# Kernel optimization log

Hardware: AMD Instinct MI355X
Metric: run time of the kernel (lower is better)

Reference implementation:

```python
import jax, jax.numpy as jnp
import numpy as np

BS, SEQ, ENC, DEC, HEADS, INTERM = 32, 2048, 512, 512, 8, 128
IH = INTERM * HEADS


def setup_inputs() -> dict:
    key = jax.random.key(0)
    ks = jax.random.split(key, 16)
    s = 0.02
    return {
        "enc": jax.random.normal(ks[0], (BS, SEQ, ENC), jnp.float32),
        "dec": jax.random.normal(ks[1], (BS, 1, DEC + ENC), jnp.float32),
        "kappa": jax.random.uniform(ks[2], (BS, 1, HEADS), jnp.float32),
        "mask": jnp.ones((BS, SEQ, 1), jnp.float32),
        "Wv": jax.random.normal(ks[3], (ENC, IH), jnp.float32) * s,
        "bv": jnp.zeros((IH,), jnp.float32),
        "Wq": jax.random.normal(ks[4], (DEC + ENC, IH), jnp.float32) * s,
        "bq": jnp.zeros((IH,), jnp.float32),
        "Wf": jax.random.normal(ks[5], (IH, HEADS), jnp.float32) * s,
        "bf": jnp.zeros((HEADS,), jnp.float32),
        "Wb": jax.random.normal(ks[6], (DEC + ENC, HEADS), jnp.float32) * s,
        "bb": jnp.zeros((HEADS,), jnp.float32),
        "Wk": jax.random.normal(ks[7], (DEC + ENC, HEADS), jnp.float32) * s,
        "bk": jnp.zeros((HEADS,), jnp.float32),
        "Wfc": jax.random.normal(ks[8], (ENC * HEADS, ENC), jnp.float32) * s,
        "bfc": jnp.zeros((ENC,), jnp.float32),
    }


def reference(enc, dec, kappa, mask, Wv, bv, Wq, bq, Wf, bf, Wb, bb, Wk, bk, Wfc, bfc):
    bs, seq_len, _ = enc.shape
    sp = jax.nn.softplus
    value = enc @ Wv + bv                      # (bs, seq, IH)
    query = dec @ Wq + bq                      # (bs, 1, IH), broadcasts over seq
    alpha = sp(jnp.tanh(query + value) @ Wf + bf) * mask   # (bs, seq, heads)
    beta = sp(dec @ Wb + bb)                   # (bs, 1, heads)
    kappa = kappa + sp(dec @ Wk + bk)          # (bs, 1, heads)
    u = jnp.arange(seq_len, dtype=enc.dtype)[None, :, None]
    score = alpha * jnp.exp(-beta * (kappa - u) ** 2)       # (bs, seq, heads)
    # weighted reduction over seq: (bs, heads, enc) then flatten in heads-major order
    context = jnp.einsum("bsh,bse->bhe", score, enc).reshape(bs, -1)
    context = context @ Wfc + bfc              # (bs, enc)
    return context[:, None, :], kappa, score
```

## Files before the change

### kernel.cpp

```cpp
#include <hip/hip_runtime.h>
#include <cstdint>
#include <cstddef>

#define BSZ    32
#define SEQL   2048
#define ENCD   512
#define DE     1024
#define NHEADS 8
#define IHD    1024

typedef unsigned short u16;
typedef __bf16 bf16x8 __attribute__((ext_vector_type(8)));
typedef float floatx4 __attribute__((ext_vector_type(4)));
typedef unsigned short u16x8 __attribute__((ext_vector_type(8)));

__device__ __forceinline__ u16 f2bf(float f) {
    unsigned int u = __float_as_uint(f);
    u = (u + 0x7FFFu + ((u >> 16) & 1u)) >> 16;
    return (u16)u;
}
__device__ __forceinline__ float bf2f(u16 v) {
    return __uint_as_float(((unsigned int)v) << 16);
}
__device__ __forceinline__ float softplus_f(float x) {
    return fmaxf(x, 0.0f) + log1pf(__expf(-fabsf(x)));
}
__device__ __forceinline__ float tanh_fast(float x) {
    const float e = __expf(2.0f * x);
    return 1.0f - 2.0f / (e + 1.0f);
}
__device__ __forceinline__ void async_cp16(u16* lds, const u16* g) {
    __builtin_amdgcn_global_load_lds(
        (const __attribute__((address_space(1))) unsigned int*)g,
        (__attribute__((address_space(3))) unsigned int*)lds, 16, 0, 0);
}

__global__ __launch_bounds__(256) void pre_kernel(
    const float* __restrict__ Wv, const float* __restrict__ Wf,
    u16* __restrict__ WvT, u16* __restrict__ wfb,
    const float* __restrict__ dec, const float* __restrict__ kappa_in,
    const float* __restrict__ Wq, const float* __restrict__ bq,
    const float* __restrict__ bv,
    const float* __restrict__ Wb, const float* __restrict__ bb,
    const float* __restrict__ Wk, const float* __restrict__ bk,
    float* __restrict__ query_ws, float* __restrict__ beta_ws,
    float* __restrict__ kappa_out)
{
    __shared__ float sh[64 * 65];
    const int bid = blockIdx.x, tid = threadIdx.x;

    if (bid < 128) {
        const int nt = bid & 15, kt = bid >> 4;
        for (int i = tid; i < 4096; i += 256) {
            const int kk = i >> 6, nn = i & 63;
            sh[kk * 65 + nn] = Wv[(size_t)(kt * 64 + kk) * IHD + nt * 64 + nn];
        }
        __syncthreads();
        for (int i = tid; i < 4096; i += 256) {
            const int nn = i >> 6, kk = i & 63;
            WvT[(size_t)(nt * 64 + nn) * 512 + kt * 64 + kk] = f2bf(sh[kk * 65 + nn]);
        }
        return;
    }
    if (bid == 128) {
        for (int i = tid; i < 8192; i += 256) {
            const int j   = i & 7;
            const int fr8 = (i >> 3) & 7;
            const int qd  = (i >> 6) & 3;
            const int ks  = (i >> 8) & 3;
            const int nn  = i >> 10;
            const int row = nn * 128 + ks * 32 + qd * 8 + j;
            wfb[i] = f2bf(Wf[row * NHEADS + fr8]);
        }
        return;
    }
    const int p = bid - 129;
    const int b = p & 31, y = p >> 5;
    float* s_dec = sh;
    float* s_red = sh + DE;
    for (int i = tid; i < DE; i += 256) s_dec[i] = dec[b * DE + i];
    __syncthreads();

    if (y < 32) {
        const int cl = tid & 31, kg = tid >> 5;
        const int col = y * 32 + cl;
        float a = 0.f;
        const float* w = Wq + col;
        #pragma unroll 4
        for (int k = kg * 128; k < kg * 128 + 128; ++k)
            a = fmaf(s_dec[k], w[(size_t)k * IHD], a);
        s_red[tid] = a;
        __syncthreads();
        if (tid < 32) {
            float s = 0.f;
            #pragma unroll
            for (int i = 0; i < 8; ++i) s += s_red[i * 32 + tid];
            query_ws[(size_t)b * IHD + col] = s + bq[col] + bv[col];
        }
    } else {
        const int h = tid & 7, kg = tid >> 3;
        float ab = 0.f, ak = 0.f;
        for (int k = kg * 32; k < kg * 32 + 32; ++k) {
            const float d = s_dec[k];
            ab = fmaf(d, Wb[k * NHEADS + h], ab);
            ak = fmaf(d, Wk[k * NHEADS + h], ak);
        }
        s_red[tid] = ab;
        __syncthreads();
        for (int off = 128; off >= 8; off >>= 1) {
            if (tid < off) s_red[tid] += s_red[tid + off];
            __syncthreads();
        }
        const float abT = (tid < 8) ? s_red[tid] : 0.f;
        __syncthreads();
        s_red[tid] = ak;
        __syncthreads();
        for (int off = 128; off >= 8; off >>= 1) {
            if (tid < off) s_red[tid] += s_red[tid + off];
            __syncthreads();
        }
        if (tid < 8) {
            beta_ws[b * NHEADS + tid]   = softplus_f(bb[tid] + abT);
            kappa_out[b * NHEADS + tid] = kappa_in[b * NHEADS + tid]
                                        + softplus_f(bk[tid] + s_red[tid]);
        }
    }
}

#define BM 128

__global__ __launch_bounds__(256, 2) void gemm_score_ctx_kernel(
    const float* __restrict__ enc, u16* __restrict__ encb,
    const u16* __restrict__ wvT,
    const u16* __restrict__ wfb2, const float* __restrict__ bf_g,
    const float* __restrict__ mask, const float* __restrict__ query_ws,
    const float* __restrict__ beta_ws, const float* __restrict__ kappa_out,
    float* __restrict__ score_out, float* __restrict__ ctx_part)
{
    __shared__ __align__(16) unsigned char smem[69632];
    u16*   tT      = (u16*)(smem + 32768);
    float* s_score = (float*)(smem + 65536);

    const int tid  = threadIdx.x;
    const int m0   = blockIdx.x * BM;
    const int b    = blockIdx.x >> 4;
    const int sc   = blockIdx.x & 15;
    const int lane = tid & 63;
    const int w    = tid >> 6;
    const int wr   = w >> 1, wc = w & 1;
    const int fr   = lane & 15, quad = lane >> 4;

    {
        const float4* src = (const float4*)enc + (size_t)m0 * 128;
        u16x8* dst = (u16x8*)(encb + (size_t)m0 * 512);
        #pragma unroll 4
        for (int i = tid; i < 8192; i += 256) {
            const float4 a = src[i * 2], b2 = src[i * 2 + 1];
            u16x8 o;
            o[0] = f2bf(a.x);  o[1] = f2bf(a.y);  o[2] = f2bf(a.z);  o[3] = f2bf(a.w);
            o[4] = f2bf(b2.x); o[5] = f2bf(b2.y); o[6] = f2bf(b2.z); o[7] = f2bf(b2.w);
            dst[i] = o;
        }
        asm volatile("s_waitcnt vmcnt(0)" ::: "memory");
        __builtin_amdgcn_sched_barrier(0);
        __builtin_amdgcn_s_barrier();
    }

    int mA[4], csA[4];
    #pragma unroll
    for (int r = 0; r < 4; ++r) {
        const int c = r * 256 + tid;
        mA[r]  = c >> 3;
        csA[r] = (c & 7) ^ (mA[r] & 7);
    }

    auto stage = [&](int bufsel, int it) {
        u16* Ab = (u16*)(smem + bufsel * 32768);
        u16* Bb = Ab + 8192;
        const int nn2 = it >> 3, kt2 = it & 7;
        const size_t aoff = (size_t)kt2 * 64;
        const size_t boff = (size_t)nn2 * (128 * 512) + (size_t)kt2 * 64;
        #pragma unroll
        for (int r = 0; r < 4; ++r) {
            async_cp16(Ab + (r * 256 + (tid & 192)) * 8,
                       encb + (size_t)(m0 + mA[r]) * 512 + aoff + csA[r] * 8);
            async_cp16(Bb + (size_t)(r * 256 + (tid & 192)) * 8,
                       wvT + (size_t)mA[r] * 512 + boff + csA[r] * 8);
        }
    };

    floatx4 acc2[2] = {};

    stage(0, 0);

    for (int nn = 0; nn < 8; ++nn) {
        const int n0 = nn * 128;
        float qv[4];
        bf16x8 wfr[4];
        floatx4 acc[4][4] = {};

        #pragma unroll
        for (int kt = 0; kt < 8; ++kt) {
            const int it = nn * 8 + kt;
            if (kt < 7 || nn < 7)
                stage((it + 1) & 1, it + 1);
            if (kt == 0) {
                #pragma unroll
                for (int nt = 0; nt < 4; ++nt)
                    qv[nt] = query_ws[(size_t)b * IHD + n0 + wc * 64 + nt * 16 + fr];
                #pragma unroll
                for (int ks = 0; ks < 4; ++ks)
                    wfr[ks] = *(const bf16x8*)&wfb2[((nn * 4 + ks) * 4 + quad) * 64
                                                    + (fr & 7) * 8];
            }
            if (kt == 7 && nn == 7) {
                asm volatile("s_waitcnt vmcnt(0)" ::: "memory");
            } else if (kt == 0) {
                asm volatile("s_waitcnt vmcnt(16)" ::: "memory");
            } else {
                asm volatile("s_waitcnt vmcnt(8)" ::: "memory");
            }
            __builtin_amdgcn_sched_barrier(0);
            __builtin_amdgcn_s_barrier();

            u16* Ab = (u16*)(smem + (it & 1) * 32768);
            u16* Bb = Ab + 8192;
            __builtin_amdgcn_s_setprio(1);
            #pragma unroll
            for (int s2 = 0; s2 < 2; ++s2) {
                bf16x8 af[4], bfr[4];
                #pragma unroll
                for (int mt = 0; mt < 4; ++mt) {
                    const int ma = wr * 64 + mt * 16 + fr;
                    const int ca = (s2 * 4 + quad) ^ (ma & 7);
                    af[mt] = *(const bf16x8*)&Ab[ma * 64 + ca * 8];
                }
                #pragma unroll
                for (int nt = 0; nt < 4; ++nt) {
                    const int nb = wc * 64 + nt * 16 + fr;
                    const int cb = (s2 * 4 + quad) ^ (nb & 7);
                    bfr[nt] = *(const bf16x8*)&Bb[nb * 64 + cb * 8];
                }
                #pragma unroll
                for (int mt = 0; mt < 4; ++mt)
                    #pragma unroll
                    for (int nt = 0; nt < 4; ++nt)
                        acc[mt][nt] = __builtin_amdgcn_mfma_f32_16x16x32_bf16(
                            af[mt], bfr[nt], acc[mt][nt], 0, 0, 0);
            }
            __builtin_amdgcn_s_setprio(0);
            __builtin_amdgcn_sched_barrier(0);
            __builtin_amdgcn_s_barrier();
        }

        #pragma unroll
        for (int mt = 0; mt < 4; ++mt) {
            #pragma unroll
            for (int nt = 0; nt < 4; ++nt) {
                const int col = wc * 64 + nt * 16 + fr;
                #pragma unroll
                for (int reg = 0; reg < 4; ++reg) {
                    const int row = wr * 64 + mt * 16 + quad * 4 + reg;
                    ((__bf16*)tT)[row * 128 + (col ^ ((row & 7) << 3))] =
                        (__bf16)tanh_fast(acc[mt][nt][reg] + qv[nt]);
                }
            }
        }
        asm volatile("s_waitcnt lgkmcnt(0)" ::: "memory");
        __builtin_amdgcn_sched_barrier(0);
        __builtin_amdgcn_s_barrier();

        #pragma unroll
        for (int t = 0; t < 2; ++t) {
            const int row = w * 32 + t * 16 + fr;
            #pragma unroll
            for (int ks = 0; ks < 4; ++ks) {
                const bf16x8 ta = *(const bf16x8*)
                    &tT[row * 128 + ((ks * 32 + quad * 8) ^ ((row & 7) << 3))];
                acc2[t] = __builtin_amdgcn_mfma_f32_16x16x32_bf16(ta, wfr[ks], acc2[t], 0, 0, 0);
            }
        }
        __builtin_amdgcn_sched_barrier(0);
        __builtin_amdgcn_s_barrier();
    }

    if (fr < NHEADS) {
        const float bfh = bf_g[fr];
        const float bet = beta_ws[b * NHEADS + fr];
        const float kap = kappa_out[b * NHEADS + fr];
        #pragma unroll
        for (int t = 0; t < 2; ++t) {
            #pragma unroll
            for (int reg = 0; reg < 4; ++reg) {
                const int row  = w * 32 + t * 16 + quad * 4 + reg;
                const int grow = m0 + row;
                const int s = grow & 2047;
                const float alpha = softplus_f(acc2[t][reg] + bfh) * mask[grow];
                const float du = kap - (float)s;
                const float v = alpha * __expf(-bet * du * du);
                score_out[(size_t)grow * NHEADS + fr] = v;
                s_score[row * NHEADS + fr] = v;
            }
        }
    }
    asm volatile("s_waitcnt lgkmcnt(0)" ::: "memory");
    __builtin_amdgcn_s_barrier();

    {
        float acc0[8] = {}, acc1[8] = {};
        const u16* ep = encb + (size_t)m0 * 512 + lane * 8;
        for (int s0 = 0; s0 < 128; s0 += 16) {
            u16x8 ev[16];
            #pragma unroll
            for (int u = 0; u < 16; ++u)
                ev[u] = *(const u16x8*)(ep + (size_t)(s0 + u) * 512);
            #pragma unroll
            for (int u = 0; u < 16; ++u) {
                const float2 sc2 = *(const float2*)&s_score[(s0 + u) * NHEADS + 2 * w];
                #pragma unroll
                for (int j = 0; j < 8; ++j) {
                    const float e = bf2f(ev[u][j]);
                    acc0[j] = fmaf(sc2.x, e, acc0[j]);
                    acc1[j] = fmaf(sc2.y, e, acc1[j]);
                }
            }
        }
        const int e8 = lane * 8;
        float* outp = ctx_part + ((size_t)sc * BSZ + b) * (NHEADS * ENCD);
        *(float4*)&outp[(2 * w + 0) * ENCD + e8]     = make_float4(acc0[0], acc0[1], acc0[2], acc0[3]);
        *(float4*)&outp[(2 * w + 0) * ENCD + e8 + 4] = make_float4(acc0[4], acc0[5], acc0[6], acc0[7]);
        *(float4*)&outp[(2 * w + 1) * ENCD + e8]     = make_float4(acc1[0], acc1[1], acc1[2], acc1[3]);
        *(float4*)&outp[(2 * w + 1) * ENCD + e8 + 4] = make_float4(acc1[4], acc1[5], acc1[6], acc1[7]);
    }
}

__global__ __launch_bounds__(256) void ctx_reduce_kernel(
    const float* __restrict__ part, float* __restrict__ ctx_ws)
{
    const int i = blockIdx.x * 256 + threadIdx.x;
    float a = 0.f;
    #pragma unroll
    for (int sc = 0; sc < 16; ++sc)
        a += part[(size_t)sc * 131072 + i];
    ctx_ws[i] = a;
}

__global__ __launch_bounds__(256) void final_kernel(
    const float* __restrict__ ctx_ws, const float* __restrict__ Wfc,
    const float* __restrict__ bfc, float* __restrict__ out_ctx)
{
    __shared__ float s_ctx[32][128];
    const int jc = blockIdx.x, ks = blockIdx.y, tid = threadIdx.x;
    const int jl = tid & 31, bg = tid >> 5;
    const int j = jc * 32 + jl;
    const int k0 = ks * 128;

    for (int i = tid; i < 32 * 128; i += 256) {
        const int bb2 = i >> 7, kk = i & 127;
        s_ctx[bb2][kk] = ctx_ws[(size_t)bb2 * (NHEADS * ENCD) + k0 + kk];
    }
    __syncthreads();

    float a0 = 0.f, a1 = 0.f, a2 = 0.f, a3 = 0.f;
    for (int kk = 0; kk < 128; ++kk) {
        const float wv = Wfc[(size_t)(k0 + kk) * ENCD + j];
        a0 = fmaf(s_ctx[bg * 4 + 0][kk], wv, a0);
        a1 = fmaf(s_ctx[bg * 4 + 1][kk], wv, a1);
        a2 = fmaf(s_ctx[bg * 4 + 2][kk], wv, a2);
        a3 = fmaf(s_ctx[bg * 4 + 3][kk], wv, a3);
    }
    const float bias = (ks == 0) ? bfc[j] : 0.0f;
    atomicAdd(&out_ctx[(bg * 4 + 0) * ENCD + j], a0 + bias);
    atomicAdd(&out_ctx[(bg * 4 + 1) * ENCD + j], a1 + bias);
    atomicAdd(&out_ctx[(bg * 4 + 2) * ENCD + j], a2 + bias);
    atomicAdd(&out_ctx[(bg * 4 + 3) * ENCD + j], a3 + bias);
}

extern "C" void kernel_launch(void* const* d_in, const int* in_sizes, int n_in,
                              void* d_out, int out_size, void* d_ws, size_t ws_size,
                              hipStream_t stream)
{
    const float* enc   = (const float*)d_in[0];
    const float* dec   = (const float*)d_in[1];
    const float* kapin = (const float*)d_in[2];
    const float* mask  = (const float*)d_in[3];
    const float* Wv    = (const float*)d_in[4];
    const float* bv    = (const float*)d_in[5];
    const float* Wq    = (const float*)d_in[6];
    const float* bq    = (const float*)d_in[7];
    const float* Wf    = (const float*)d_in[8];
    const float* bf    = (const float*)d_in[9];
    const float* Wb    = (const float*)d_in[10];
    const float* bb    = (const float*)d_in[11];
    const float* Wk    = (const float*)d_in[12];
    const float* bk    = (const float*)d_in[13];
    const float* Wfc   = (const float*)d_in[14];
    const float* bfc   = (const float*)d_in[15];

    float* out       = (float*)d_out;
    float* out_ctx   = out;
    float* out_kappa = out + 16384;
    float* out_score = out + 16640;

    char* w = (char*)d_ws;
    u16*   enc_bf   = (u16*)w;
    float* ctx_part = (float*)(w + 67108864);
    u16*   wvT      = (u16*)(w + 75497472);
    float* q_ws     = (float*)(w + 76546048);
    float* beta_ws  = (float*)(w + 76677120);
    float* ctx_ws   = (float*)(w + 76678144);
    u16*   wfb      = (u16*)(w + 77202432);

    hipMemsetAsync(out_ctx, 0, 16384 * sizeof(float), stream);

    pre_kernel<<<dim3(128 + 1 + 1056), dim3(256), 0, stream>>>(
        Wv, Wf, wvT, wfb,
        dec, kapin, Wq, bq, bv, Wb, bb, Wk, bk, q_ws, beta_ws, out_kappa);

    gemm_score_ctx_kernel<<<dim3((BSZ * SEQL) / BM), dim3(256), 0, stream>>>(
        enc, enc_bf, wvT, wfb, bf, mask, q_ws, beta_ws, out_kappa,
        out_score, ctx_part);

    ctx_reduce_kernel<<<dim3(512), dim3(256), 0, stream>>>(ctx_part, ctx_ws);

    final_kernel<<<dim3(16, 32), dim3(256), 0, stream>>>(
        ctx_ws, Wfc, bfc, out_ctx);
}
```

Before: 396.0 us.

## Enlarge fused GEMM block tile to 256x256 with 512 threads

Doubles the per-block M tile to 256 rows and the N chunk to 256 columns, with 8 waves per block and a 4x8 MFMA accumulator tile per wave. LDS grows to about 136KB to hold double-buffered A/B tiles and a 256-row tanh tile. The aim is to reuse each loaded Wv and enc tile across more output and to halve the grid to 256 blocks. The tanh epilogue now runs in two halves, with only one column group of waves writing at a time, and per-thread register pressure rises sharply. The context reduction splits the waves across two 128-row halves so the partial-sum layout stays the same.

```diff
diff --git a/kernel.cpp b/kernel.cpp
--- a/kernel.cpp
+++ b/kernel.cpp
@@ -127,9 +127,9 @@
     }
 }
 
-#define BM 128
-
-__global__ __launch_bounds__(256, 2) void gemm_score_ctx_kernel(
+#define BM 256
+
+__global__ __launch_bounds__(512, 1) void gemm_score_ctx_kernel(
     const float* __restrict__ enc, u16* __restrict__ encb,
     const u16* __restrict__ wvT,
     const u16* __restrict__ wfb2, const float* __restrict__ bf_g,
@@ -137,14 +137,14 @@
     const float* __restrict__ beta_ws, const float* __restrict__ kappa_out,
     float* __restrict__ score_out, float* __restrict__ ctx_part)
 {
-    __shared__ __align__(16) unsigned char smem[69632];
-    u16*   tT      = (u16*)(smem + 32768);
-    float* s_score = (float*)(smem + 65536);
+    __shared__ __align__(16) unsigned char smem[139264];
+    u16*   tT      = (u16*)(smem + 65536);
+    float* s_score = (float*)(smem + 131072);
 
     const int tid  = threadIdx.x;
     const int m0   = blockIdx.x * BM;
-    const int b    = blockIdx.x >> 4;
-    const int sc   = blockIdx.x & 15;
+    const int b    = blockIdx.x >> 3;
+    const int scb  = blockIdx.x & 7;
     const int lane = tid & 63;
     const int w    = tid >> 6;
     const int wr   = w >> 1, wc = w & 1;
@@ -154,7 +154,7 @@
         const float4* src = (const float4*)enc + (size_t)m0 * 128;
         u16x8* dst = (u16x8*)(encb + (size_t)m0 * 512);
         #pragma unroll 4
-        for (int i = tid; i < 8192; i += 256) {
+        for (int i = tid; i < 16384; i += 512) {
             const float4 a = src[i * 2], b2 = src[i * 2 + 1];
             u16x8 o;
             o[0] = f2bf(a.x);  o[1] = f2bf(a.y);  o[2] = f2bf(a.z);  o[3] = f2bf(a.w);
@@ -169,66 +169,50 @@
     int mA[4], csA[4];
     #pragma unroll
     for (int r = 0; r < 4; ++r) {
-        const int c = r * 256 + tid;
+        const int c = r * 512 + tid;
         mA[r]  = c >> 3;
         csA[r] = (c & 7) ^ (mA[r] & 7);
     }
 
-    auto stage = [&](int bufsel, int it) {
-        u16* Ab = (u16*)(smem + bufsel * 32768);
-        u16* Bb = Ab + 8192;
-        const int nn2 = it >> 3, kt2 = it & 7;
+    auto stage = [&](int sel, int pp2, int kt2) {
+        u16* Ab = (u16*)(smem + sel * 65536);
+        u16* Bb = Ab + 16384;
         const size_t aoff = (size_t)kt2 * 64;
-        const size_t boff = (size_t)nn2 * (128 * 512) + (size_t)kt2 * 64;
+        const size_t boff = (size_t)pp2 * (256 * 512) + (size_t)kt2 * 64;
         #pragma unroll
         for (int r = 0; r < 4; ++r) {
-            async_cp16(Ab + (r * 256 + (tid & 192)) * 8,
+            async_cp16(Ab + (r * 512 + (tid & 448)) * 8,
                        encb + (size_t)(m0 + mA[r]) * 512 + aoff + csA[r] * 8);
-            async_cp16(Bb + (size_t)(r * 256 + (tid & 192)) * 8,
+            async_cp16(Bb + (size_t)(r * 512 + (tid & 448)) * 8,
                        wvT + (size_t)mA[r] * 512 + boff + csA[r] * 8);
         }
     };
 
     floatx4 acc2[2] = {};
 
-    stage(0, 0);
-
-    for (int nn = 0; nn < 8; ++nn) {
-        const int n0 = nn * 128;
-        float qv[4];
-        bf16x8 wfr[4];
-        floatx4 acc[4][4] = {};
+    stage(0, 0, 0);
+
+    for (int pp = 0; pp < 4; ++pp) {
+        floatx4 acc[4][8] = {};
 
         #pragma unroll
         for (int kt = 0; kt < 8; ++kt) {
-            const int it = nn * 8 + kt;
-            if (kt < 7 || nn < 7)
-                stage((it + 1) & 1, it + 1);
-            if (kt == 0) {
-                #pragma unroll
-                for (int nt = 0; nt < 4; ++nt)
-                    qv[nt] = query_ws[(size_t)b * IHD + n0 + wc * 64 + nt * 16 + fr];
-                #pragma unroll
-                for (int ks = 0; ks < 4; ++ks)
-                    wfr[ks] = *(const bf16x8*)&wfb2[((nn * 4 + ks) * 4 + quad) * 64
-                                                    + (fr & 7) * 8];
-            }
-            if (kt == 7 && nn == 7) {
+            if (kt < 7)       stage((kt + 1) & 1, pp, kt + 1);
+            else if (pp < 3)  stage(0, pp + 1, 0);
+            if (kt == 7 && pp == 3) {
                 asm volatile("s_waitcnt vmcnt(0)" ::: "memory");
-            } else if (kt == 0) {
-                asm volatile("s_waitcnt vmcnt(16)" ::: "memory");
             } else {
                 asm volatile("s_waitcnt vmcnt(8)" ::: "memory");
             }
             __builtin_amdgcn_sched_barrier(0);
             __builtin_amdgcn_s_barrier();
 
-            u16* Ab = (u16*)(smem + (it & 1) * 32768);
-            u16* Bb = Ab + 8192;
+            const u16* Ab = (const u16*)(smem + (kt & 1) * 65536);
+            const u16* Bb = Ab + 16384;
             __builtin_amdgcn_s_setprio(1);
             #pragma unroll
             for (int s2 = 0; s2 < 2; ++s2) {
-                bf16x8 af[4], bfr[4];
+                bf16x8 af[4], bfr[8];
                 #pragma unroll
                 for (int mt = 0; mt < 4; ++mt) {
                     const int ma = wr * 64 + mt * 16 + fr;
@@ -236,15 +220,15 @@
                     af[mt] = *(const bf16x8*)&Ab[ma * 64 + ca * 8];
                 }
                 #pragma unroll
-                for (int nt = 0; nt < 4; ++nt) {
-                    const int nb = wc * 64 + nt * 16 + fr;
+                for (int nt = 0; nt < 8; ++nt) {
+                    const int nb = wc * 128 + nt * 16 + fr;
                     const int cb = (s2 * 4 + quad) ^ (nb & 7);
                     bfr[nt] = *(const bf16x8*)&Bb[nb * 64 + cb * 8];
                 }
                 #pragma unroll
                 for (int mt = 0; mt < 4; ++mt)
                     #pragma unroll
-                    for (int nt = 0; nt < 4; ++nt)
+                    for (int nt = 0; nt < 8; ++nt)
                         acc[mt][nt] = __builtin_amdgcn_mfma_f32_16x16x32_bf16(
                             af[mt], bfr[nt], acc[mt][nt], 0, 0, 0);
             }
@@ -254,34 +238,50 @@
         }
 
         #pragma unroll
-        for (int mt = 0; mt < 4; ++mt) {
-            #pragma unroll
-            for (int nt = 0; nt < 4; ++nt) {
-                const int col = wc * 64 + nt * 16 + fr;
-                #pragma unroll
-                for (int reg = 0; reg < 4; ++reg) {
-                    const int row = wr * 64 + mt * 16 + quad * 4 + reg;
-                    ((__bf16*)tT)[row * 128 + (col ^ ((row & 7) << 3))] =
-                        (__bf16)tanh_fast(acc[mt][nt][reg] + qv[nt]);
+        for (int s = 0; s < 2; ++s) {
+            const int n0 = pp * 256 + s * 128;
+            if (wc == s) {
+                float qv[8];
+                #pragma unroll
+                for (int nt = 0; nt < 8; ++nt)
+                    qv[nt] = query_ws[(size_t)b * IHD + n0 + nt * 16 + fr];
+                #pragma unroll
+                for (int mt = 0; mt < 4; ++mt) {
+                    #pragma unroll
+                    for (int nt = 0; nt < 8; ++nt) {
+                        const int col = nt * 16 + fr;
+                        #pragma unroll
+                        for (int reg = 0; reg < 4; ++reg) {
+                            const int row = wr * 64 + mt * 16 + quad * 4 + reg;
+                            ((__bf16*)tT)[row * 128 + (col ^ ((row & 7) << 3))] =
+                                (__bf16)tanh_fast(acc[mt][nt][reg] + qv[nt]);
+                        }
+                    }
                 }
             }
-        }
-        asm volatile("s_waitcnt lgkmcnt(0)" ::: "memory");
-        __builtin_amdgcn_sched_barrier(0);
-        __builtin_amdgcn_s_barrier();
-
-        #pragma unroll
-        for (int t = 0; t < 2; ++t) {
-            const int row = w * 32 + t * 16 + fr;
-            #pragma unroll
-            for (int ks = 0; ks < 4; ++ks) {
-                const bf16x8 ta = *(const bf16x8*)
-                    &tT[row * 128 + ((ks * 32 + quad * 8) ^ ((row & 7) << 3))];
-                acc2[t] = __builtin_amdgcn_mfma_f32_16x16x32_bf16(ta, wfr[ks], acc2[t], 0, 0, 0);
-            }
-        }
-        __builtin_amdgcn_sched_barrier(0);
-        __builtin_amdgcn_s_barrier();
+            asm volatile("s_waitcnt lgkmcnt(0)" ::: "memory");
+            __builtin_amdgcn_sched_barrier(0);
+            __builtin_amdgcn_s_barrier();
+
+            bf16x8 wfr[4];
+            #pragma unroll
+            for (int ks = 0; ks < 4; ++ks)
+                wfr[ks] = *(const bf16x8*)&wfb2[(((pp * 2 + s) * 4 + ks) * 4
+                                                 + quad) * 64 + (fr & 7) * 8];
+            #pragma unroll
+            for (int t = 0; t < 2; ++t) {
+                const int row = w * 32 + t * 16 + fr;
+                #pragma unroll
+                for (int ks = 0; ks < 4; ++ks) {
+                    const bf16x8 ta = *(const bf16x8*)
+                        &tT[row * 128 + ((ks * 32 + quad * 8) ^ ((row & 7) << 3))];
+                    acc2[t] = __builtin_amdgcn_mfma_f32_16x16x32_bf16(
+                        ta, wfr[ks], acc2[t], 0, 0, 0);
+                }
+            }
+            __builtin_amdgcn_sched_barrier(0);
+            __builtin_amdgcn_s_barrier();
+        }
     }
 
     if (fr < NHEADS) {
@@ -307,8 +307,9 @@
     __builtin_amdgcn_s_barrier();
 
     {
+        const int hp = w & 3, sh = w >> 2;
         float acc0[8] = {}, acc1[8] = {};
-        const u16* ep = encb + (size_t)m0 * 512 + lane * 8;
+        const u16* ep = encb + (size_t)(m0 + sh * 128) * 512 + lane * 8;
         for (int s0 = 0; s0 < 128; s0 += 16) {
             u16x8 ev[16];
             #pragma unroll
@@ -316,7 +317,8 @@
                 ev[u] = *(const u16x8*)(ep + (size_t)(s0 + u) * 512);
             #pragma unroll
             for (int u = 0; u < 16; ++u) {
-                const float2 sc2 = *(const float2*)&s_score[(s0 + u) * NHEADS + 2 * w];
+                const float2 sc2 = *(const float2*)
+                    &s_score[(sh * 128 + s0 + u) * NHEADS + 2 * hp];
                 #pragma unroll
                 for (int j = 0; j < 8; ++j) {
                     const float e = bf2f(ev[u][j]);
@@ -326,11 +328,12 @@
             }
         }
         const int e8 = lane * 8;
-        float* outp = ctx_part + ((size_t)sc * BSZ + b) * (NHEADS * ENCD);
-        *(float4*)&outp[(2 * w + 0) * ENCD + e8]     = make_float4(acc0[0], acc0[1], acc0[2], acc0[3]);
-        *(float4*)&outp[(2 * w + 0) * ENCD + e8 + 4] = make_float4(acc0[4], acc0[5], acc0[6], acc0[7]);
-        *(float4*)&outp[(2 * w + 1) * ENCD + e8]     = make_float4(acc1[0], acc1[1], acc1[2], acc1[3]);
-        *(float4*)&outp[(2 * w + 1) * ENCD + e8 + 4] = make_float4(acc1[4], acc1[5], acc1[6], acc1[7]);
+        const int sc2i = scb * 2 + sh;
+        float* outp = ctx_part + ((size_t)sc2i * BSZ + b) * (NHEADS * ENCD);
+        *(float4*)&outp[(2 * hp + 0) * ENCD + e8]     = make_float4(acc0[0], acc0[1], acc0[2], acc0[3]);
+        *(float4*)&outp[(2 * hp + 0) * ENCD + e8 + 4] = make_float4(acc0[4], acc0[5], acc0[6], acc0[7]);
+        *(float4*)&outp[(2 * hp + 1) * ENCD + e8]     = make_float4(acc1[0], acc1[1], acc1[2], acc1[3]);
+        *(float4*)&outp[(2 * hp + 1) * ENCD + e8 + 4] = make_float4(acc1[4], acc1[5], acc1[6], acc1[7]);
     }
 }
 
@@ -417,7 +420,7 @@
         Wv, Wf, wvT, wfb,
         dec, kapin, Wq, bq, bv, Wb, bb, Wk, bk, q_ws, beta_ws, out_kappa);
 
-    gemm_score_ctx_kernel<<<dim3((BSZ * SEQL) / BM), dim3(256), 0, stream>>>(
+    gemm_score_ctx_kernel<<<dim3((BSZ * SEQL) / BM), dim3(512), 0, stream>>>(
         enc, enc_bf, wvT, wfb, bf, mask, q_ws, beta_ws, out_kappa,
         out_score, ctx_part);
 
```

New measurement: 627.1 us. +58.3%, slower.
